# Performance work log

Hardware: AMD Instinct MI355X
Metric: run time of the kernel (lower is better)

## Reference

```python
import jax, jax.numpy as jnp
import numpy as np


def setup_inputs() -> dict:
    key = jax.random.key(0)
    k1, k2 = jax.random.split(key)
    x = jax.random.normal(k1, (32, 128, 64, 64), dtype=jnp.float32)
    weight = jax.random.normal(k2, (256, 128, 3, 3), dtype=jnp.float32)
    return {"x": x, "weight": weight}


def reference(x, weight):
    # Batched VALID cross-correlation, stride 1 (same math as the triple loop
    # of single-channel conv2d calls summed over in_channels).
    # x: [B, Cin, H, W]; weight: [Cout, Cin, k, k] -> out: [B, Cout, H-k+1, W-k+1]
    return jax.lax.conv_general_dilated(
        x, weight,
        window_strides=(1, 1),
        padding="VALID",
        dimension_numbers=("NCHW", "OIHW", "NCHW"),
    )
```

## Files before the change

### kernel.cpp

```cpp
#include <hip/hip_runtime.h>


using bf16x8 = __attribute__((ext_vector_type(8))) __bf16;
using f32x4  = __attribute__((ext_vector_type(4))) float;
using f32x16 = __attribute__((ext_vector_type(16))) float;

constexpr int CIN  = 128;
constexpr int HW   = 64;
constexpr int COUT = 256;
constexpr int OW   = 62;
constexpr int NS   = 62 * 62;
constexpr int NTOT = 32 * NS;
constexpr int KTOT = 9 * CIN;
constexpr int BN = 128, BK = 32;
constexpr int NSTEP = KTOT / BK;
constexpr int NWG = NTOT / BN;

constexpr size_t AP_BYTES = (size_t)COUT * KTOT * 2;
constexpr size_t XP_BYTES = (size_t)32 * HW * HW * CIN * 2;
constexpr size_t WS_NEEDED = AP_BYTES + XP_BYTES;

constexpr int SBUF = 24576;
constexpr int BOFF = 16384;

__device__ __forceinline__ unsigned short f2bf(float f) {
  unsigned u = __float_as_uint(f);
  u += 0x7fffu + ((u >> 16) & 1u);
  return (unsigned short)(u >> 16);
}
__device__ __forceinline__ unsigned pack2(float a, float b) {
  return (unsigned)f2bf(a) | ((unsigned)f2bf(b) << 16);
}

__device__ __forceinline__ void gld16(const void* g, void* l) {
  __builtin_amdgcn_global_load_lds(
      (const __attribute__((address_space(1))) unsigned int*)g,
      (__attribute__((address_space(3))) unsigned int*)l, 16, 0, 0);
}


__global__ __launch_bounds__(256)
void prepack_w(const float* __restrict__ w, unsigned* __restrict__ ap32) {
  const int idx = blockIdx.x * 256 + threadIdx.x;
  const int co  = idx / 576;
  const int k2  = idx - co * 576;
  const int k   = k2 * 2;
  const int tap = k >> 7;
  const int ci  = k & 127;
  const float v0 = w[(co * 128 + ci) * 9 + tap];
  const float v1 = w[(co * 128 + ci + 1) * 9 + tap];
  ap32[idx] = pack2(v0, v1);
}

__global__ __launch_bounds__(256)
void prepack_x(const float* __restrict__ x, unsigned* __restrict__ xp32) {
  const int bh = blockIdx.x;
  const int b  = bh >> 6, h = bh & 63;
  const int t  = threadIdx.x;
  const int c  = t & 63;
  const int w0 = (t >> 6) * 16;

  const float* p0 = x + (((size_t)(b * 128 + 2 * c) * HW) + h) * HW + w0;
  const float* p1 = p0 + (size_t)HW * HW;
  float r0[16], r1[16];
#pragma unroll
  for (int j = 0; j < 4; ++j) {
    *reinterpret_cast<float4*>(&r0[j * 4]) = reinterpret_cast<const float4*>(p0)[j];
    *reinterpret_cast<float4*>(&r1[j * 4]) = reinterpret_cast<const float4*>(p1)[j];
  }
  unsigned* o = xp32 + ((size_t)bh * HW + w0) * 64 + c;
#pragma unroll
  for (int j = 0; j < 16; ++j)
    o[j * 64] = pack2(r0[j], r1[j]);
}


__global__ __launch_bounds__(256, 2)
void conv_main(const unsigned short* __restrict__ Ap,
               const unsigned short* __restrict__ Xp,
               float* __restrict__ out) {
  __shared__ __align__(16) char lds[3 * SBUF];

  const int tid  = threadIdx.x;
  const int lane = tid & 63;
  const int wid  = tid >> 6;
  const int wm   = wid >> 1;
  const int wn   = wid & 1;

  int wg;
  {
    const int f = blockIdx.x;
    constexpr int q = NWG / 8, r = NWG % 8;
    const int xc = f & 7, p = f >> 3;
    wg = (xc < r ? xc * (q + 1) : r * (q + 1) + (xc - r) * q) + p;
  }
  const int n_base = wg * BN;

  const int lrow2 = ((lane >> 3) << 1) + ((lane >> 2) & 1);
  const int g8    = ((lane & 3) ^ ((lane >> 3) & 3)) * 8;
  int aoff[4];
#pragma unroll
  for (int q = 0; q < 4; ++q) {
    const int row = (wid * 4 + q) * 16 + lrow2;
    aoff[q] = row * KTOT + g8;
  }
  unsigned xoff[2];
#pragma unroll
  for (int q = 0; q < 2; ++q) {
    const int rn = (wid * 2 + q) * 16 + lrow2;
    const unsigned n  = n_base + rn;
    const unsigned bi = n / NS;
    const unsigned s0 = n - bi * NS;
    const unsigned oh = s0 / OW;
    const unsigned ww = s0 - oh * OW;
    xoff[q] = ((bi * HW + oh) * HW + ww) * CIN + g8;
  }

  const int cl = lane & 31;
  const int gl = lane >> 5;
  const int q4 = (cl >> 1) & 3;
  const int sw0 = ((gl)     ^ q4) * 16;
  const int sw1 = ((2 + gl) ^ q4) * 16;
  const int ABASE = ((wm * 64 + (cl >> 1)) * 128) + (cl & 1) * 64;
  const int BBASE = BOFF + ((wn * 32 + (cl >> 1)) * 128) + (cl & 1) * 64;

  f32x16 acc[4][2] = {};

  auto STAGE = [&](int t, char* dst) {
    const int tap = t >> 2;
    const int kh  = tap / 3;
    const int kw  = tap - kh * 3;
    const int ak  = t * BK;
    const int xk  = (kh * HW + kw) * CIN + (t & 3) * BK;
#pragma unroll
    for (int q = 0; q < 4; ++q)
      gld16(Ap + aoff[q] + ak, dst + (wid * 4 + q) * 1024);
#pragma unroll
    for (int q = 0; q < 2; ++q)
      gld16(Xp + xoff[q] + xk, dst + BOFF + (wid * 2 + q) * 1024);
  };

  STAGE(0, lds);
  STAGE(1, lds + SBUF);

#pragma unroll
  for (int t = 0; t < NSTEP; ++t) {
    const char* cur = lds + (t % 3) * SBUF;
    if (t < NSTEP - 1) asm volatile("s_waitcnt vmcnt(6)" ::: "memory");
    else               asm volatile("s_waitcnt vmcnt(0)" ::: "memory");
    __builtin_amdgcn_s_barrier();
    __builtin_amdgcn_sched_barrier(0);
    if (t + 2 < NSTEP) STAGE(t + 2, lds + ((t + 2) % 3) * SBUF);

#pragma unroll
    for (int kf = 0; kf < 2; ++kf) {
      const int sw = kf ? sw1 : sw0;
      bf16x8 a[4], b[2];
#pragma unroll
      for (int mt = 0; mt < 4; ++mt)
        a[mt] = *reinterpret_cast<const bf16x8*>(cur + ABASE + mt * 2048 + sw);
#pragma unroll
      for (int nt = 0; nt < 2; ++nt)
        b[nt] = *reinterpret_cast<const bf16x8*>(cur + BBASE + nt * 2048 + sw);

      __builtin_amdgcn_s_setprio(1);
#pragma unroll
      for (int mt = 0; mt < 4; ++mt)
#pragma unroll
        for (int nt = 0; nt < 2; ++nt)
          acc[mt][nt] = __builtin_amdgcn_mfma_f32_32x32x16_bf16(
              a[mt], b[nt], acc[mt][nt], 0, 0, 0);
      __builtin_amdgcn_s_setprio(0);
    }
  }

#pragma unroll
  for (int mt = 0; mt < 4; ++mt)
#pragma unroll
    for (int nt = 0; nt < 2; ++nt) {
      const unsigned n  = n_base + wn * 64 + nt * 32 + cl;
      const unsigned b2 = n / NS;
      const unsigned s2 = n - b2 * NS;
      float* op = out + (size_t)b2 * (COUT * NS) + s2
                      + (size_t)(wm * 128 + mt * 32 + gl * 4) * NS;
#pragma unroll
      for (int r = 0; r < 16; ++r)
        op[((r & 3) + 8 * (r >> 2)) * NS] = acc[mt][nt][r];
    }
}


__global__ __launch_bounds__(256)
void conv_fallback(const float* __restrict__ x, const float* __restrict__ w,
                   float* __restrict__ out) {
  __shared__ __align__(16) unsigned short As[128 * 32];
  __shared__ __align__(16) unsigned short Bs[128 * 32];

  const int t    = threadIdx.x;
  const int lane = t & 63;
  const int wid  = t >> 6;
  const int wm   = wid >> 1;
  const int wn   = wid & 1;
  const int co_base = blockIdx.x * 128;
  const int n_base  = blockIdx.y * 128;

  const int bn  = t & 127;
  const int bg0 = t >> 7;
  const unsigned n0   = n_base + bn;
  const unsigned bidx = n0 / NS;
  const unsigned s0   = n0 - bidx * NS;
  const unsigned oh   = s0 / OW;
  const unsigned ow   = s0 - oh * OW;
  const float* xb = x + (bidx * (CIN * HW * HW) + oh * HW + ow);

  const int am  = t & 127;
  const int ag0 = (t >> 7) * 2;
  const float* wb = w + (co_base + am) * KTOT;

  f32x4 acc[4][4] = {};

  for (int ks = 0; ks < 36; ++ks) {
    const int tap = ks >> 2;
    const int ci0 = (ks & 3) * 32;
    const int kh  = tap / 3;
    const int kw  = tap - kh * 3;
    const int xo  = kh * HW + kw;

    float av[2][8], bv[2][8];
#pragma unroll
    for (int gi = 0; gi < 2; ++gi) {
      const int g = ag0 + gi;
#pragma unroll
      for (int j = 0; j < 8; ++j)
        av[gi][j] = wb[(ci0 + g * 8 + j) * 9 + tap];
    }
#pragma unroll
    for (int gi = 0; gi < 2; ++gi) {
      const int g = bg0 + gi * 2;
#pragma unroll
      for (int j = 0; j < 8; ++j)
        bv[gi][j] = xb[xo + (ci0 + g * 8 + j) * (HW * HW)];
    }

    __syncthreads();

#pragma unroll
    for (int gi = 0; gi < 2; ++gi) {
      const int g = ag0 + gi;
      uint4 pv;
      pv.x = pack2(av[gi][0], av[gi][1]);
      pv.y = pack2(av[gi][2], av[gi][3]);
      pv.z = pack2(av[gi][4], av[gi][5]);
      pv.w = pack2(av[gi][6], av[gi][7]);
      *reinterpret_cast<uint4*>(&As[am * 32 + ((g ^ ((am >> 1) & 3)) << 3)]) = pv;
    }
#pragma unroll
    for (int gi = 0; gi < 2; ++gi) {
      const int g = bg0 + gi * 2;
      uint4 pv;
      pv.x = pack2(bv[gi][0], bv[gi][1]);
      pv.y = pack2(bv[gi][2], bv[gi][3]);
      pv.z = pack2(bv[gi][4], bv[gi][5]);
      pv.w = pack2(bv[gi][6], bv[gi][7]);
      *reinterpret_cast<uint4*>(&Bs[bn * 32 + ((g ^ ((bn >> 1) & 3)) << 3)]) = pv;
    }

    __syncthreads();

    bf16x8 af[4], bfr[4];
    const int g = lane >> 4;
#pragma unroll
    for (int mi = 0; mi < 4; ++mi) {
      const int m = wm * 64 + mi * 16 + (lane & 15);
      af[mi] = *reinterpret_cast<const bf16x8*>(&As[m * 32 + ((g ^ ((m >> 1) & 3)) << 3)]);
    }
#pragma unroll
    for (int ni = 0; ni < 4; ++ni) {
      const int nn = wn * 64 + ni * 16 + (lane & 15);
      bfr[ni] = *reinterpret_cast<const bf16x8*>(&Bs[nn * 32 + ((g ^ ((nn >> 1) & 3)) << 3)]);
    }
#pragma unroll
    for (int mi = 0; mi < 4; ++mi)
#pragma unroll
      for (int ni = 0; ni < 4; ++ni)
        acc[mi][ni] = __builtin_amdgcn_mfma_f32_16x16x32_bf16(af[mi], bfr[ni],
                                                              acc[mi][ni], 0, 0, 0);
  }

#pragma unroll
  for (int ni = 0; ni < 4; ++ni) {
    const unsigned n  = n_base + wn * 64 + ni * 16 + (lane & 15);
    const unsigned b2 = n / NS;
    const unsigned s2 = n - b2 * NS;
    float* op = out + (size_t)b2 * (COUT * NS) + s2
                    + (size_t)(co_base + wm * 64 + (lane >> 4) * 4) * NS;
#pragma unroll
    for (int mi = 0; mi < 4; ++mi)
#pragma unroll
      for (int r = 0; r < 4; ++r)
        op[(mi * 16 + r) * NS] = acc[mi][ni][r];
  }
}

extern "C" void kernel_launch(void* const* d_in, const int* in_sizes, int n_in,
                              void* d_out, int out_size, void* d_ws, size_t ws_size,
                              hipStream_t stream) {
  const float* x = (const float*)d_in[0];
  const float* w = (const float*)d_in[1];
  float* out = (float*)d_out;

  if (ws_size >= WS_NEEDED) {
    unsigned* ap32 = (unsigned*)d_ws;
    unsigned short* Ap = (unsigned short*)d_ws;
    unsigned short* Xp = (unsigned short*)((char*)d_ws + AP_BYTES);
    unsigned* xp32 = (unsigned*)Xp;
    prepack_w<<<576, 256, 0, stream>>>(w, ap32);
    prepack_x<<<32 * HW, 256, 0, stream>>>(x, xp32);
    conv_main<<<dim3(NWG), 256, 0, stream>>>(Ap, Xp, out);
  } else {
    conv_fallback<<<dim3(2, NTOT / 128), 256, 0, stream>>>(x, w, out);
  }
}
```

Measured before the change: 110.9 us.

## Tile output by two-row panels and reuse staged input halo across all 3x3 taps

Each workgroup now covers two full output rows (124 pixels) of one image. For each 32-channel chunk it stages a 4-row input halo into LDS once, then reads the B operand for all nine taps from that halo, rather than reloading shifted input rows from global memory per tap. The K loop is reordered to channel-chunk-major and uses separate double buffers for weights and halo. In exchange, 4 of 128 N columns per tile do no useful work, LDS use rises to 64KB, and the waitcnt/barrier schedule is more complex, which may cut occupancy.

```diff
diff --git a/kernel.cpp b/kernel.cpp
--- a/kernel.cpp
+++ b/kernel.cpp
@@ -12,16 +12,12 @@
 constexpr int NS   = 62 * 62;
 constexpr int NTOT = 32 * NS;
 constexpr int KTOT = 9 * CIN;
-constexpr int BN = 128, BK = 32;
-constexpr int NSTEP = KTOT / BK;
-constexpr int NWG = NTOT / BN;
+constexpr int BNR  = 124;
+constexpr int NPAN = NTOT / BNR;
 
 constexpr size_t AP_BYTES = (size_t)COUT * KTOT * 2;
 constexpr size_t XP_BYTES = (size_t)32 * HW * HW * CIN * 2;
 constexpr size_t WS_NEEDED = AP_BYTES + XP_BYTES;
-
-constexpr int SBUF = 24576;
-constexpr int BOFF = 16384;
 
 __device__ __forceinline__ unsigned short f2bf(float f) {
   unsigned u = __float_as_uint(f);
@@ -79,7 +75,7 @@
 void conv_main(const unsigned short* __restrict__ Ap,
                const unsigned short* __restrict__ Xp,
                float* __restrict__ out) {
-  __shared__ __align__(16) char lds[3 * SBUF];
+  __shared__ __align__(16) char lds[65536];
 
   const int tid  = threadIdx.x;
   const int lane = tid & 63;
@@ -87,33 +83,30 @@
   const int wm   = wid >> 1;
   const int wn   = wid & 1;
 
-  int wg;
-  {
-    const int f = blockIdx.x;
-    constexpr int q = NWG / 8, r = NWG % 8;
-    const int xc = f & 7, p = f >> 3;
-    wg = (xc < r ? xc * (q + 1) : r * (q + 1) + (xc - r) * q) + p;
-  }
-  const int n_base = wg * BN;
+  int wg; { const int f = blockIdx.x; wg = (f & 7) * 124 + (f >> 3); }
+  const int bi  = wg / 31;
+  const int oh0 = (wg - bi * 31) * 2;
+  const int n_base = wg * BNR;
+  (void)n_base;
 
   const int lrow2 = ((lane >> 3) << 1) + ((lane >> 2) & 1);
-  const int g8    = ((lane & 3) ^ ((lane >> 3) & 3)) * 8;
+  const int g8a   = ((lane & 3) ^ ((lane >> 3) & 3)) * 8;
   int aoff[4];
 #pragma unroll
   for (int q = 0; q < 4; ++q) {
     const int row = (wid * 4 + q) * 16 + lrow2;
-    aoff[q] = row * KTOT + g8;
-  }
-  unsigned xoff[2];
-#pragma unroll
-  for (int q = 0; q < 2; ++q) {
-    const int rn = (wid * 2 + q) * 16 + lrow2;
-    const unsigned n  = n_base + rn;
-    const unsigned bi = n / NS;
-    const unsigned s0 = n - bi * NS;
-    const unsigned oh = s0 / OW;
-    const unsigned ww = s0 - oh * OW;
-    xoff[q] = ((bi * HW + oh) * HW + ww) * CIN + g8;
+    aoff[q] = row * KTOT + g8a;
+  }
+
+  int hsrc[4];
+#pragma unroll
+  for (int q = 0; q < 4; ++q) {
+    const int line = (wid * 4 + q) * 8 + (lane >> 3);
+    const int r    = line >> 5;
+    const int owp  = line & 31;
+    const int ow   = owp * 2 + ((lane >> 2) & 1);
+    hsrc[q] = ((bi * 64 + oh0 + r) * HW + ow) * CIN
+            + (((lane & 3) ^ (line & 3)) << 3);
   }
 
   const int cl = lane & 31;
@@ -122,71 +115,98 @@
   const int sw0 = ((gl)     ^ q4) * 16;
   const int sw1 = ((2 + gl) ^ q4) * 16;
   const int ABASE = ((wm * 64 + (cl >> 1)) * 128) + (cl & 1) * 64;
-  const int BBASE = BOFF + ((wn * 32 + (cl >> 1)) * 128) + (cl & 1) * 64;
+
+  int drf[2], owf[2];
+#pragma unroll
+  for (int nt = 0; nt < 2; ++nt) {
+    int ln = wn * 64 + nt * 32 + cl;
+    if (ln > BNR - 1) ln = BNR - 1;
+    drf[nt] = (ln >= 62) ? 1 : 0;
+    owf[nt] = ln - drf[nt] * 62;
+  }
 
   f32x16 acc[4][2] = {};
 
-  auto STAGE = [&](int t, char* dst) {
-    const int tap = t >> 2;
-    const int kh  = tap / 3;
-    const int kw  = tap - kh * 3;
-    const int ak  = t * BK;
-    const int xk  = (kh * HW + kw) * CIN + (t & 3) * BK;
+  char* ab[2] = { lds,          lds + 16384 };
+  char* hb[2] = { lds + 32768,  lds + 49152 };
+
+  auto STAGE_A = [&](int s, char* dst) {
+    const int cc = s / 9, tap = s % 9;
+    const int ak = tap * CIN + cc * 32;
 #pragma unroll
     for (int q = 0; q < 4; ++q)
       gld16(Ap + aoff[q] + ak, dst + (wid * 4 + q) * 1024);
-#pragma unroll
-    for (int q = 0; q < 2; ++q)
-      gld16(Xp + xoff[q] + xk, dst + BOFF + (wid * 2 + q) * 1024);
   };
-
-  STAGE(0, lds);
-  STAGE(1, lds + SBUF);
-
-#pragma unroll
-  for (int t = 0; t < NSTEP; ++t) {
-    const char* cur = lds + (t % 3) * SBUF;
-    if (t < NSTEP - 1) asm volatile("s_waitcnt vmcnt(6)" ::: "memory");
-    else               asm volatile("s_waitcnt vmcnt(0)" ::: "memory");
+  auto STAGE_H = [&](int cc, char* dst) {
+#pragma unroll
+    for (int q = 0; q < 4; ++q)
+      gld16(Xp + hsrc[q] + cc * 32, dst + (wid * 4 + q) * 1024);
+  };
+
+  STAGE_H(0, hb[0]);
+  STAGE_A(0, ab[0]);
+
+#pragma unroll
+  for (int s = 0; s < 36; ++s) {
+    const int c = s / 9, tap = s % 9;
+    const int kh = tap / 3, kw = tap - kh * 3;
+
+    if (s == 5 || s == 14 || s == 23)
+      asm volatile("s_waitcnt vmcnt(4)" ::: "memory");
+    else
+      asm volatile("s_waitcnt vmcnt(0)" ::: "memory");
     __builtin_amdgcn_s_barrier();
-    __builtin_amdgcn_sched_barrier(0);
-    if (t + 2 < NSTEP) STAGE(t + 2, lds + ((t + 2) % 3) * SBUF);
-
-#pragma unroll
-    for (int kf = 0; kf < 2; ++kf) {
-      const int sw = kf ? sw1 : sw0;
-      bf16x8 a[4], b[2];
-#pragma unroll
-      for (int mt = 0; mt < 4; ++mt)
-        a[mt] = *reinterpret_cast<const bf16x8*>(cur + ABASE + mt * 2048 + sw);
-#pragma unroll
-      for (int nt = 0; nt < 2; ++nt)
-        b[nt] = *reinterpret_cast<const bf16x8*>(cur + BBASE + nt * 2048 + sw);
-
-      __builtin_amdgcn_s_setprio(1);
+
+    if (s + 1 < 36) STAGE_A(s + 1, ab[(s + 1) & 1]);
+    if (tap == 4 && c < 3) STAGE_H(c + 1, hb[(c + 1) & 1]);
+
+    const char* A = ab[s & 1];
+    const char* H = hb[c & 1];
+
+    bf16x8 a[4][2], b[2][2];
+#pragma unroll
+    for (int mt = 0; mt < 4; ++mt) {
+      a[mt][0] = *reinterpret_cast<const bf16x8*>(A + ABASE + mt * 2048 + sw0);
+      a[mt][1] = *reinterpret_cast<const bf16x8*>(A + ABASE + mt * 2048 + sw1);
+    }
+#pragma unroll
+    for (int nt = 0; nt < 2; ++nt) {
+      const int owp = owf[nt] + kw;
+      const int l2  = owp >> 1;
+      const int line = (drf[nt] + kh) * 32 + l2;
+      const int base = line * 128 + (owp & 1) * 64;
+      const int k3   = line & 3;
+      b[nt][0] = *reinterpret_cast<const bf16x8*>(H + base + (((gl)     ^ k3) * 16));
+      b[nt][1] = *reinterpret_cast<const bf16x8*>(H + base + (((2 + gl) ^ k3) * 16));
+    }
+
+    __builtin_amdgcn_s_setprio(1);
+#pragma unroll
+    for (int kf = 0; kf < 2; ++kf)
 #pragma unroll
       for (int mt = 0; mt < 4; ++mt)
 #pragma unroll
         for (int nt = 0; nt < 2; ++nt)
           acc[mt][nt] = __builtin_amdgcn_mfma_f32_32x32x16_bf16(
-              a[mt], b[nt], acc[mt][nt], 0, 0, 0);
-      __builtin_amdgcn_s_setprio(0);
-    }
-  }
-
-#pragma unroll
-  for (int mt = 0; mt < 4; ++mt)
-#pragma unroll
-    for (int nt = 0; nt < 2; ++nt) {
-      const unsigned n  = n_base + wn * 64 + nt * 32 + cl;
-      const unsigned b2 = n / NS;
-      const unsigned s2 = n - b2 * NS;
-      float* op = out + (size_t)b2 * (COUT * NS) + s2
-                      + (size_t)(wm * 128 + mt * 32 + gl * 4) * NS;
+              a[mt][kf], b[nt][kf], acc[mt][nt], 0, 0, 0);
+    __builtin_amdgcn_s_setprio(0);
+  }
+
+#pragma unroll
+  for (int nt = 0; nt < 2; ++nt) {
+    const int ln = wn * 64 + nt * 32 + cl;
+    if (ln >= BNR) continue;
+    const int dr = (ln >= 62) ? 1 : 0;
+    const int ow = ln - dr * 62;
+    float* op = out + (size_t)bi * (COUT * NS) + (oh0 + dr) * OW + ow;
+#pragma unroll
+    for (int mt = 0; mt < 4; ++mt) {
+      float* op2 = op + (size_t)(wm * 128 + mt * 32 + gl * 4) * NS;
 #pragma unroll
       for (int r = 0; r < 16; ++r)
-        op[((r & 3) + 8 * (r >> 2)) * NS] = acc[mt][nt][r];
-    }
+        op2[((r & 3) + 8 * (r >> 2)) * NS] = acc[mt][nt][r];
+    }
+  }
 }
 
 
@@ -316,7 +336,7 @@
     unsigned* xp32 = (unsigned*)Xp;
     prepack_w<<<576, 256, 0, stream>>>(w, ap32);
     prepack_x<<<32 * HW, 256, 0, stream>>>(x, xp32);
-    conv_main<<<dim3(NWG), 256, 0, stream>>>(Ap, Xp, out);
+    conv_main<<<dim3(NPAN), 256, 0, stream>>>(Ap, Xp, out);
   } else {
     conv_fallback<<<dim3(2, NTOT / 128), 256, 0, stream>>>(x, w, out);
   }
```

Result: slower. 114.7 us (+3.4%).

## Enlarge conv GEMM tile to 256x256 with 512 threads and double-buffered BK=64

Applied to the files above, without the earlier changes.

Reworks the main implicit-GEMM kernel to use 8 waves per block, covering all 256 output channels and 256 output pixels per block, instead of 4 waves over 128 pixels. The K loop now runs 18 steps of 64 in two 32-wide halves, with separate double-buffered A and B regions in 128KB of LDS. Loads for the next step are issued partway through the MFMA work. The partial last block is handled by clamping indices and skipping out-of-range stores. The larger tile raises reuse of the staged weight and activation data and halves per-step barrier overhead. The cost is that the large LDS allocation limits residency to one block per CU.

```diff
diff --git a/kernel.cpp b/kernel.cpp
--- a/kernel.cpp
+++ b/kernel.cpp
@@ -12,16 +12,13 @@
 constexpr int NS   = 62 * 62;
 constexpr int NTOT = 32 * NS;
 constexpr int KTOT = 9 * CIN;
-constexpr int BN = 128, BK = 32;
-constexpr int NSTEP = KTOT / BK;
-constexpr int NWG = NTOT / BN;
+constexpr int BN = 256;
+constexpr int NT = 18;
+constexpr int NBLK = (NTOT + BN - 1) / BN;
 
 constexpr size_t AP_BYTES = (size_t)COUT * KTOT * 2;
 constexpr size_t XP_BYTES = (size_t)32 * HW * HW * CIN * 2;
 constexpr size_t WS_NEEDED = AP_BYTES + XP_BYTES;
-
-constexpr int SBUF = 24576;
-constexpr int BOFF = 16384;
 
 __device__ __forceinline__ unsigned short f2bf(float f) {
   unsigned u = __float_as_uint(f);
@@ -31,7 +28,6 @@
 __device__ __forceinline__ unsigned pack2(float a, float b) {
   return (unsigned)f2bf(a) | ((unsigned)f2bf(b) << 16);
 }
-
 __device__ __forceinline__ void gld16(const void* g, void* l) {
   __builtin_amdgcn_global_load_lds(
       (const __attribute__((address_space(1))) unsigned int*)g,
@@ -47,9 +43,7 @@
   const int k   = k2 * 2;
   const int tap = k >> 7;
   const int ci  = k & 127;
-  const float v0 = w[(co * 128 + ci) * 9 + tap];
-  const float v1 = w[(co * 128 + ci + 1) * 9 + tap];
-  ap32[idx] = pack2(v0, v1);
+  ap32[idx] = pack2(w[(co * 128 + ci) * 9 + tap], w[(co * 128 + ci + 1) * 9 + tap]);
 }
 
 __global__ __launch_bounds__(256)
@@ -59,7 +53,6 @@
   const int t  = threadIdx.x;
   const int c  = t & 63;
   const int w0 = (t >> 6) * 16;
-
   const float* p0 = x + (((size_t)(b * 128 + 2 * c) * HW) + h) * HW + w0;
   const float* p1 = p0 + (size_t)HW * HW;
   float r0[16], r1[16];
@@ -75,40 +68,37 @@
 }
 
 
-__global__ __launch_bounds__(256, 2)
+__global__ __launch_bounds__(512, 2)
 void conv_main(const unsigned short* __restrict__ Ap,
                const unsigned short* __restrict__ Xp,
                float* __restrict__ out) {
-  __shared__ __align__(16) char lds[3 * SBUF];
+  __shared__ __align__(16) char lds[131072];
 
   const int tid  = threadIdx.x;
   const int lane = tid & 63;
   const int wid  = tid >> 6;
-  const int wm   = wid >> 1;
-  const int wn   = wid & 1;
+  const int wm   = wid & 1;
+  const int wn   = wid >> 1;
 
   int wg;
   {
     const int f = blockIdx.x;
-    constexpr int q = NWG / 8, r = NWG % 8;
-    const int xc = f & 7, p = f >> 3;
+    constexpr int q = NBLK / 8, r = NBLK % 8;
+    const int xc = f % 8, p = f / 8;
     wg = (xc < r ? xc * (q + 1) : r * (q + 1) + (xc - r) * q) + p;
   }
   const int n_base = wg * BN;
 
   const int lrow2 = ((lane >> 3) << 1) + ((lane >> 2) & 1);
   const int g8    = ((lane & 3) ^ ((lane >> 3) & 3)) * 8;
-  int aoff[4];
-#pragma unroll
-  for (int q = 0; q < 4; ++q) {
-    const int row = (wid * 4 + q) * 16 + lrow2;
-    aoff[q] = row * KTOT + g8;
-  }
+  int aoff[2];
   unsigned xoff[2];
 #pragma unroll
   for (int q = 0; q < 2; ++q) {
-    const int rn = (wid * 2 + q) * 16 + lrow2;
-    const unsigned n  = n_base + rn;
+    const int rr = (wid * 2 + q) * 16 + lrow2;
+    aoff[q] = rr * KTOT + g8;
+    unsigned n = n_base + rr;
+    if (n >= NTOT) n = NTOT - 1;
     const unsigned bi = n / NS;
     const unsigned s0 = n - bi * NS;
     const unsigned oh = s0 / OW;
@@ -121,56 +111,76 @@
   const int q4 = (cl >> 1) & 3;
   const int sw0 = ((gl)     ^ q4) * 16;
   const int sw1 = ((2 + gl) ^ q4) * 16;
-  const int ABASE = ((wm * 64 + (cl >> 1)) * 128) + (cl & 1) * 64;
-  const int BBASE = BOFF + ((wn * 32 + (cl >> 1)) * 128) + (cl & 1) * 64;
+  const int ABASE = (wm * 64 + (cl >> 1)) * 128 + (cl & 1) * 64;
+  const int BBASE = (wn * 32 + (cl >> 1)) * 128 + (cl & 1) * 64;
 
   f32x16 acc[4][2] = {};
 
-  auto STAGE = [&](int t, char* dst) {
-    const int tap = t >> 2;
-    const int kh  = tap / 3;
-    const int kw  = tap - kh * 3;
-    const int ak  = t * BK;
-    const int xk  = (kh * HW + kw) * CIN + (t & 3) * BK;
-#pragma unroll
-    for (int q = 0; q < 4; ++q)
-      gld16(Ap + aoff[q] + ak, dst + (wid * 4 + q) * 1024);
+  auto STAGE_A = [&](int t, int kh) {
+    char* dst = lds + (t & 1) * 32768 + kh * 16384;
+    const int ak = t * 64 + kh * 32;
 #pragma unroll
     for (int q = 0; q < 2; ++q)
-      gld16(Xp + xoff[q] + xk, dst + BOFF + (wid * 2 + q) * 1024);
+      gld16(Ap + aoff[q] + ak, dst + (wid * 2 + q) * 1024);
   };
-
-  STAGE(0, lds);
-  STAGE(1, lds + SBUF);
-
-#pragma unroll
-  for (int t = 0; t < NSTEP; ++t) {
-    const char* cur = lds + (t % 3) * SBUF;
-    if (t < NSTEP - 1) asm volatile("s_waitcnt vmcnt(6)" ::: "memory");
-    else               asm volatile("s_waitcnt vmcnt(0)" ::: "memory");
-    __builtin_amdgcn_s_barrier();
-    __builtin_amdgcn_sched_barrier(0);
-    if (t + 2 < NSTEP) STAGE(t + 2, lds + ((t + 2) % 3) * SBUF);
-
-#pragma unroll
-    for (int kf = 0; kf < 2; ++kf) {
-      const int sw = kf ? sw1 : sw0;
-      bf16x8 a[4], b[2];
-#pragma unroll
-      for (int mt = 0; mt < 4; ++mt)
-        a[mt] = *reinterpret_cast<const bf16x8*>(cur + ABASE + mt * 2048 + sw);
-#pragma unroll
-      for (int nt = 0; nt < 2; ++nt)
-        b[nt] = *reinterpret_cast<const bf16x8*>(cur + BBASE + nt * 2048 + sw);
-
-      __builtin_amdgcn_s_setprio(1);
-#pragma unroll
-      for (int mt = 0; mt < 4; ++mt)
-#pragma unroll
-        for (int nt = 0; nt < 2; ++nt)
-          acc[mt][nt] = __builtin_amdgcn_mfma_f32_32x32x16_bf16(
-              a[mt], b[nt], acc[mt][nt], 0, 0, 0);
-      __builtin_amdgcn_s_setprio(0);
+  auto STAGE_B = [&](int t, int kh) {
+    char* dst = lds + 65536 + (t & 1) * 32768 + kh * 16384;
+    const int q32 = t * 2 + kh;
+    const int tap = q32 >> 2, ci0 = (q32 & 3) * 32;
+    const int kh3 = tap / 3, kw3 = tap - kh3 * 3;
+    const int xk  = (kh3 * HW + kw3) * CIN + ci0;
+#pragma unroll
+    for (int q = 0; q < 2; ++q)
+      gld16(Xp + xoff[q] + xk, dst + (wid * 2 + q) * 1024);
+  };
+
+  STAGE_A(0, 0); STAGE_B(0, 0); STAGE_A(0, 1); STAGE_B(0, 1);
+
+#pragma unroll
+  for (int t = 0; t < NT; ++t) {
+    const char* Ab = lds + (t & 1) * 32768;
+    const char* Bb = lds + 65536 + (t & 1) * 32768;
+#pragma unroll
+    for (int kh = 0; kh < 2; ++kh) {
+      if (kh == 0 || t < NT - 1)
+        asm volatile("s_waitcnt vmcnt(4)" ::: "memory");
+      else
+        asm volatile("s_waitcnt vmcnt(0)" ::: "memory");
+      __builtin_amdgcn_s_barrier();
+      __builtin_amdgcn_sched_barrier(0);
+      if (t + 1 < NT) STAGE_A(t + 1, kh);
+
+      const char* Abh = Ab + kh * 16384;
+      const char* Bbh = Bb + kh * 16384;
+
+      bf16x8 b[2][2];
+#pragma unroll
+      for (int nt = 0; nt < 2; ++nt) {
+        b[nt][0] = *reinterpret_cast<const bf16x8*>(Bbh + BBASE + nt * 2048 + sw0);
+        b[nt][1] = *reinterpret_cast<const bf16x8*>(Bbh + BBASE + nt * 2048 + sw1);
+      }
+#pragma unroll
+      for (int mh = 0; mh < 2; ++mh) {
+        if (mh == 1 && t + 1 < NT) STAGE_B(t + 1, kh);
+        bf16x8 a[2][2];
+#pragma unroll
+        for (int j = 0; j < 2; ++j) {
+          a[j][0] = *reinterpret_cast<const bf16x8*>(Abh + ABASE + (mh * 2 + j) * 2048 + sw0);
+          a[j][1] = *reinterpret_cast<const bf16x8*>(Abh + ABASE + (mh * 2 + j) * 2048 + sw1);
+        }
+        asm volatile("s_waitcnt lgkmcnt(0)" ::: "memory");
+        __builtin_amdgcn_sched_barrier(0);
+        __builtin_amdgcn_s_setprio(1);
+#pragma unroll
+        for (int kf = 0; kf < 2; ++kf)
+#pragma unroll
+          for (int j = 0; j < 2; ++j)
+#pragma unroll
+            for (int nt = 0; nt < 2; ++nt)
+              acc[mh * 2 + j][nt] = __builtin_amdgcn_mfma_f32_32x32x16_bf16(
+                  a[j][kf], b[nt][kf], acc[mh * 2 + j][nt], 0, 0, 0);
+        __builtin_amdgcn_s_setprio(0);
+      }
     }
   }
 
@@ -178,7 +188,8 @@
   for (int mt = 0; mt < 4; ++mt)
 #pragma unroll
     for (int nt = 0; nt < 2; ++nt) {
-      const unsigned n  = n_base + wn * 64 + nt * 32 + cl;
+      const unsigned n = n_base + wn * 64 + nt * 32 + cl;
+      if (n >= NTOT) continue;
       const unsigned b2 = n / NS;
       const unsigned s2 = n - b2 * NS;
       float* op = out + (size_t)b2 * (COUT * NS) + s2
@@ -316,7 +327,7 @@
     unsigned* xp32 = (unsigned*)Xp;
     prepack_w<<<576, 256, 0, stream>>>(w, ap32);
     prepack_x<<<32 * HW, 256, 0, stream>>>(x, xp32);
-    conv_main<<<dim3(NWG), 256, 0, stream>>>(Ap, Xp, out);
+    conv_main<<<dim3(NBLK), 512, 0, stream>>>(Ap, Xp, out);
   } else {
     conv_fallback<<<dim3(2, NTOT / 128), 256, 0, stream>>>(x, w, out);
   }
```

After: 114.8 us. +3.5%, slower.
